# Kernel optimization log

Hardware: AMD Instinct MI355X
Metric: run time of the kernel (lower is better)

The kernel has to match this reference:

```python
import jax, jax.numpy as jnp
import numpy as np

N_TOKENS = 16384
MODEL_DIM = 2048
NUM_EXPERTS = 16
TOP_K = 2
CAPACITY_FACTOR = 1.0
NUM_SPLIT = 2  # os.environ 'num_split' default in source


def setup_inputs() -> dict:
    key = jax.random.key(0)
    kx, kw = jax.random.split(key)
    x = jax.random.normal(kx, (N_TOKENS, MODEL_DIM), dtype=jnp.float32)
    # kaiming_normal_ on Linear weight: std = sqrt(2 / fan_in)
    wg = jax.random.normal(kw, (NUM_EXPERTS, MODEL_DIM), dtype=jnp.float32) * np.float32(np.sqrt(2.0 / MODEL_DIM))
    return {"x": x, "wg": wg}


def _loss_compute(logits):
    gates = jax.nn.softmax(logits, axis=1)              # [N, E]
    num_experts = logits.shape[1]
    indices1_s = jnp.argmax(gates, axis=1)              # [N]
    mask1 = jax.nn.one_hot(indices1_s, num_experts, dtype=gates.dtype)
    me = jnp.mean(gates, axis=0)
    ce = jnp.mean(mask1, axis=0)
    l_aux = jnp.sum(me * ce) * num_experts
    return l_aux, indices1_s, gates


def _dispatch_fix_capacity(gates, k, capacity_factor, num_split):
    # gates is detached in the original (torch .detach())
    gates = jax.lax.stop_gradient(gates)
    n, e = gates.shape
    capacity = int(k * n // e * capacity_factor) // num_split * num_split
    values, topk_idx = jax.lax.top_k(gates, k)          # [N, k]
    weights = values
    flat_experts = topk_idx.reshape(-1)                 # [N*k]
    order = jnp.argsort(flat_experts)                   # stable sort by expert id
    experts_sorted = flat_experts[order]
    token_ids = jnp.repeat(jnp.arange(n, dtype=jnp.int32), k)[order]
    # position of each routed token within its expert's run
    counts = jax.ops.segment_sum(jnp.ones_like(flat_experts, dtype=jnp.int32), flat_experts, num_segments=e)
    starts = jnp.cumsum(counts) - counts                # exclusive prefix sum
    pos = jnp.arange(n * k, dtype=jnp.int32) - starts[experts_sorted]
    # fixed-capacity index table, -1 = empty slot; overflow tokens dropped
    ind = jnp.full((e, capacity), -1, dtype=jnp.int32)
    ind = ind.at[experts_sorted, pos].set(token_ids, mode="drop")  # pos>=capacity dropped
    indices = ind.reshape(-1)                           # [E*capacity], expert-major
    mask = indices >= 0
    expert_ids = jnp.repeat(jnp.arange(e, dtype=gates.dtype), capacity)
    return weights, indices, expert_ids, mask


def reference(x, wg):
    logits = jnp.einsum("nd,ed->ne", x, wg)             # Linear, no bias
    l_aux, _indices1, gates = _loss_compute(logits)
    weights, indices, expert_ids, mask = _dispatch_fix_capacity(
        gates, TOP_K, CAPACITY_FACTOR, NUM_SPLIT)
    return l_aux, weights, indices, expert_ids
```

## Files before the change

### kernel.cpp

```cpp
#include <hip/hip_runtime.h>
#include <hip/hip_bf16.h>
#include <stdint.h>

#define N_TOKENS    16384
#define MODEL_DIM   2048
#define NUM_EXPERTS 16
#define CAPACITY    2048
#define NBLK2       512
#define NBLK        256
#define GBLK        512
#define W_OFF       1
#define IDX_OFF     (1 + 2 * N_TOKENS)
#define EID_OFF     (IDX_OFF + NUM_EXPERTS * CAPACITY)

#define SC_E01    0
#define SC_CNTH   16384
#define SC_CEH    32768
#define SC_START  49152
#define SC_TOT    57344
#define SC_ME     57408

#define DPPX(v, ctrl) __int_as_float(__builtin_amdgcn_update_dpp(             \
    0, __float_as_int(v), (ctrl), 0xF, 0xF, true))
#define SWZ(v, off) __int_as_float(__builtin_amdgcn_ds_swizzle(               \
    __float_as_int(v), (off)))

__global__ __launch_bounds__(512) void k_logits(
    const float* __restrict__ x, const float* __restrict__ wg,
    float* __restrict__ out, uint8_t* __restrict__ ws)
{
  __shared__ float part[8][32][17];
  const int tid = threadIdx.x;
  const int b = blockIdx.x;
  const int l = tid & 63;
  const int kr = tid >> 6;
  const int kb = kr * 256 + l * 4;

  float4 w[16];
#pragma unroll
  for (int e = 0; e < NUM_EXPERTS; ++e)
    w[e] = *reinterpret_cast<const float4*>(wg + e * MODEL_DIM + kb);

  const float* xp = x + (size_t)(b * 32) * MODEL_DIM + kb;
  float4 xva = *reinterpret_cast<const float4*>(xp);

  const bool h0 = l & 1, h1 = l & 2, h2 = l & 4, h3 = l & 8;

  for (int t = 0; t < 32; ++t) {
    float4 xvb;
    if (t < 31)
      xvb = *reinterpret_cast<const float4*>(xp + (size_t)(t + 1) * MODEL_DIM);

    float cur[16];
#pragma unroll
    for (int e = 0; e < NUM_EXPERTS; ++e)
      cur[e] = xva.x * w[e].x + xva.y * w[e].y + xva.z * w[e].z + xva.w * w[e].w;

#pragma unroll
    for (int r = 0; r < 8; ++r) {
      float k = h0 ? cur[2 * r + 1] : cur[2 * r];
      float o = h0 ? cur[2 * r]     : cur[2 * r + 1];
      cur[r] = k + DPPX(o, 0xB1);
    }
#pragma unroll
    for (int r = 0; r < 4; ++r) {
      float k = h1 ? cur[2 * r + 1] : cur[2 * r];
      float o = h1 ? cur[2 * r]     : cur[2 * r + 1];
      cur[r] = k + DPPX(o, 0x4E);
    }
#pragma unroll
    for (int r = 0; r < 2; ++r) {
      float k = h2 ? cur[2 * r + 1] : cur[2 * r];
      float o = h2 ? cur[2 * r]     : cur[2 * r + 1];
      cur[r] = k + SWZ(o, 0x101F);
    }
    float v;
    {
      float k = h3 ? cur[1] : cur[0];
      float o = h3 ? cur[0] : cur[1];
      v = k + SWZ(o, 0x201F);
    }
    v += SWZ(v, 0x401F);
    v += __shfl_xor(v, 32, 64);
    if (l < NUM_EXPERTS) part[kr][t][l] = v;
    xva = xvb;
  }
  __syncthreads();

  if (tid < 32) {
    const int tg = b * 32 + tid;
    float logit[NUM_EXPERTS];
#pragma unroll
    for (int e = 0; e < NUM_EXPERTS; ++e) {
      float s = part[0][tid][e];
#pragma unroll
      for (int k2 = 1; k2 < 8; ++k2) s += part[k2][tid][e];
      logit[e] = s;
    }

    float m = logit[0];
#pragma unroll
    for (int e = 1; e < NUM_EXPERTS; e++) m = fmaxf(m, logit[e]);
    float gg[NUM_EXPERTS]; float z = 0.f;
#pragma unroll
    for (int e = 0; e < NUM_EXPERTS; e++) { gg[e] = expf(logit[e] - m); z += gg[e]; }
    float inv = 1.f / z;
#pragma unroll
    for (int e = 0; e < NUM_EXPERTS; e++) gg[e] *= inv;

    float v1 = gg[0], v2 = -1.f; int e1 = 0, e2 = 0;
#pragma unroll
    for (int e = 1; e < NUM_EXPERTS; e++) {
      if (gg[e] > v1) { v2 = v1; e2 = e1; v1 = gg[e]; e1 = e; }
      else if (gg[e] > v2) { v2 = gg[e]; e2 = e; }
    }
    out[W_OFF + 2 * tg]     = v1;
    out[W_OFF + 2 * tg + 1] = v2;
    ws[SC_E01 + tg] = (uint8_t)(e1 | (e2 << 4));

    int mycount = 0, myce = 0;
    for (int e = 0; e < NUM_EXPERTS; e++) {
      unsigned long long m1 = __ballot(e1 == e);
      unsigned long long m2 = __ballot(e2 == e);
      if (tid == e) { mycount = __popcll(m1 | m2); myce = __popcll(m1); }
    }
    if (tid < NUM_EXPERTS) {
      reinterpret_cast<uint16_t*>(ws + SC_CNTH)[tid * NBLK2 + b] = (uint16_t)mycount;
      reinterpret_cast<uint16_t*>(ws + SC_CEH)[tid * NBLK2 + b] = (uint16_t)myce;
    }

#pragma unroll
    for (int e = 0; e < NUM_EXPERTS; e++) {
      gg[e] += __shfl_xor(gg[e], 1, 64);
      gg[e] += __shfl_xor(gg[e], 2, 64);
      gg[e] += __shfl_xor(gg[e], 4, 64);
      gg[e] += __shfl_xor(gg[e], 8, 64);
      gg[e] += __shfl_xor(gg[e], 16, 64);
    }
    if (tid == 0) {
      float* mp = reinterpret_cast<float*>(ws + SC_ME);
#pragma unroll
      for (int e = 0; e < NUM_EXPERTS; e++) mp[b * NUM_EXPERTS + e] = gg[e];
    }
  }
}

__global__ __launch_bounds__(256) void k_finish(
    uint8_t* __restrict__ ws, float* __restrict__ out) {
  const uint16_t* cnth = reinterpret_cast<const uint16_t*>(ws + SC_CNTH);
  uint16_t* starts = reinterpret_cast<uint16_t*>(ws + SC_START);
  uint16_t* totw = reinterpret_cast<uint16_t*>(ws + SC_TOT);
  __shared__ int gs[NUM_EXPERTS][16];
  __shared__ int gstart[NUM_EXPERTS][17];
  __shared__ float sme[NUM_EXPERTS][17];
  __shared__ int sce[NUM_EXPERTS][17];
  const int tid = threadIdx.x;
  const int e = tid >> 4, grp = tid & 15;
  int s = 0;
  for (int hc = grp * 32; hc < grp * 32 + 32; hc++) s += cnth[e * NBLK2 + hc];
  gs[e][grp] = s;
  {
    const float* mepart = reinterpret_cast<const float*>(ws + SC_ME);
    const uint16_t* ceh = reinterpret_cast<const uint16_t*>(ws + SC_CEH);
    float ms = 0.f; int cs = 0;
    for (int k = grp; k < NBLK2; k += 16) {
      ms += mepart[k * NUM_EXPERTS + e];
      cs += ceh[e * NBLK2 + k];
    }
    sme[e][grp] = ms; sce[e][grp] = cs;
  }
  __syncthreads();
  if (tid < NUM_EXPERTS) {
    int run = 0;
    for (int g2 = 0; g2 < 16; g2++) { gstart[tid][g2] = run; run += gs[tid][g2]; }
  }
  __syncthreads();
  int run = gstart[e][grp];
  for (int c = grp * 16; c < grp * 16 + 16; c++) {
    starts[e * NBLK + c] = (uint16_t)run;
    run += cnth[e * NBLK2 + 2 * c] + cnth[e * NBLK2 + 2 * c + 1];
  }
  if (grp == 15) totw[e] = (uint16_t)run;
  if (tid < NUM_EXPERTS) {
    float ssum = 0.f; int ce = 0;
    for (int g2 = 0; g2 < 16; g2++) { ssum += sme[tid][g2]; ce += sce[tid][g2]; }
    float prod = (ssum * (1.0f / N_TOKENS)) * ((float)ce * (1.0f / N_TOKENS));
    prod += __shfl_xor(prod, 1, 64);
    prod += __shfl_xor(prod, 2, 64);
    prod += __shfl_xor(prod, 4, 64);
    prod += __shfl_xor(prod, 8, 64);
    if (tid == 0) out[0] = prod * (float)NUM_EXPERTS;
  }
}

__global__ __launch_bounds__(192) void k_scatter_fill(
    const uint8_t* __restrict__ ws, float* __restrict__ out) {
  const uint16_t* starts = reinterpret_cast<const uint16_t*>(ws + SC_START);
  const uint16_t* totw = reinterpret_cast<const uint16_t*>(ws + SC_TOT);
  const int tid = threadIdx.x;
  const int b = blockIdx.x;
  if (tid < 64) {
    const int t = b * 64 + tid;
    const int v = ws[SC_E01 + t];
    const int e1 = v & 15, e2 = v >> 4;
    const unsigned long long below = (1ull << tid) - 1ull;
    int p1 = CAPACITY, p2 = CAPACITY;
    for (int e = 0; e < NUM_EXPERTS; e++) {
      unsigned long long m = __ballot(e1 == e) | __ballot(e2 == e);
      int r = __popcll(m & below);
      int sbase = (int)starts[e * NBLK + b];
      if (e1 == e) p1 = sbase + r;
      if (e2 == e) p2 = sbase + r;
    }
    float tf = (float)t;
    if ((unsigned)p1 < (unsigned)CAPACITY) out[IDX_OFF + e1 * CAPACITY + p1] = tf;
    if ((unsigned)p2 < (unsigned)CAPACITY) out[IDX_OFF + e2 * CAPACITY + p2] = tf;
  } else {
    const int slot = b * 128 + (tid - 64);
    const int e = slot >> 11;
    const int p = slot & (CAPACITY - 1);
    if (p >= (int)totw[e]) out[IDX_OFF + slot] = -1.0f;
    out[EID_OFF + slot] = (float)e;
  }
}

extern "C" void kernel_launch(void* const* d_in, const int* in_sizes, int n_in,
                              void* d_out, int out_size, void* d_ws, size_t ws_size,
                              hipStream_t stream) {
  const float* x  = (const float*)d_in[0];
  const float* wg = (const float*)d_in[1];
  float* out = (float*)d_out;
  uint8_t* ws = (uint8_t*)d_ws;

  k_logits<<<GBLK, 512, 0, stream>>>(x, wg, out, ws);
  k_finish<<<1, 256, 0, stream>>>(ws, out);
  k_scatter_fill<<<NBLK, 192, 0, stream>>>(ws, out);
}
```

Before: 52.11 us.

## Fuse finish into scatter kernel with per-block prefix recompute, deepen x prefetch

Removes the single-block k_finish launch. Each scatter block now recomputes its own per-expert exclusive prefix and totals from the histogram counts, and an extra block 256 computes the aux loss. This cuts a kernel launch and a serial dependency stage, at the cost of redundant histogram reads in every block. The logits kernel also prefetches x two rows ahead instead of one, and replaces one ds_swizzle with a DPP row-shift for the cross-8-lane reduction step.

```diff
diff --git a/kernel.cpp b/kernel.cpp
--- a/kernel.cpp
+++ b/kernel.cpp
@@ -16,9 +16,7 @@
 #define SC_E01    0
 #define SC_CNTH   16384
 #define SC_CEH    32768
-#define SC_START  49152
-#define SC_TOT    57344
-#define SC_ME     57408
+#define SC_ME     49152
 
 #define DPPX(v, ctrl) __int_as_float(__builtin_amdgcn_update_dpp(             \
     0, __float_as_int(v), (ctrl), 0xF, 0xF, true))
@@ -43,13 +41,14 @@
 
   const float* xp = x + (size_t)(b * 32) * MODEL_DIM + kb;
   float4 xva = *reinterpret_cast<const float4*>(xp);
+  float4 xvb = *reinterpret_cast<const float4*>(xp + MODEL_DIM);
 
   const bool h0 = l & 1, h1 = l & 2, h2 = l & 4, h3 = l & 8;
 
   for (int t = 0; t < 32; ++t) {
-    float4 xvb;
-    if (t < 31)
-      xvb = *reinterpret_cast<const float4*>(xp + (size_t)(t + 1) * MODEL_DIM);
+    float4 xvc;
+    if (t < 30)
+      xvc = *reinterpret_cast<const float4*>(xp + (size_t)(t + 2) * MODEL_DIM);
 
     float cur[16];
 #pragma unroll
@@ -78,12 +77,12 @@
     {
       float k = h3 ? cur[1] : cur[0];
       float o = h3 ? cur[0] : cur[1];
-      v = k + SWZ(o, 0x201F);
+      v = k + DPPX(o, 0x128);
     }
     v += SWZ(v, 0x401F);
     v += __shfl_xor(v, 32, 64);
     if (l < NUM_EXPERTS) part[kr][t][l] = v;
-    xva = xvb;
+    xva = xvb; xvb = xvc;
   }
   __syncthreads();
 
@@ -145,60 +144,58 @@
   }
 }
 
-__global__ __launch_bounds__(256) void k_finish(
-    uint8_t* __restrict__ ws, float* __restrict__ out) {
-  const uint16_t* cnth = reinterpret_cast<const uint16_t*>(ws + SC_CNTH);
-  uint16_t* starts = reinterpret_cast<uint16_t*>(ws + SC_START);
-  uint16_t* totw = reinterpret_cast<uint16_t*>(ws + SC_TOT);
-  __shared__ int gs[NUM_EXPERTS][16];
-  __shared__ int gstart[NUM_EXPERTS][17];
-  __shared__ float sme[NUM_EXPERTS][17];
-  __shared__ int sce[NUM_EXPERTS][17];
-  const int tid = threadIdx.x;
-  const int e = tid >> 4, grp = tid & 15;
-  int s = 0;
-  for (int hc = grp * 32; hc < grp * 32 + 32; hc++) s += cnth[e * NBLK2 + hc];
-  gs[e][grp] = s;
-  {
-    const float* mepart = reinterpret_cast<const float*>(ws + SC_ME);
-    const uint16_t* ceh = reinterpret_cast<const uint16_t*>(ws + SC_CEH);
-    float ms = 0.f; int cs = 0;
-    for (int k = grp; k < NBLK2; k += 16) {
-      ms += mepart[k * NUM_EXPERTS + e];
-      cs += ceh[e * NBLK2 + k];
-    }
-    sme[e][grp] = ms; sce[e][grp] = cs;
-  }
-  __syncthreads();
-  if (tid < NUM_EXPERTS) {
-    int run = 0;
-    for (int g2 = 0; g2 < 16; g2++) { gstart[tid][g2] = run; run += gs[tid][g2]; }
-  }
-  __syncthreads();
-  int run = gstart[e][grp];
-  for (int c = grp * 16; c < grp * 16 + 16; c++) {
-    starts[e * NBLK + c] = (uint16_t)run;
-    run += cnth[e * NBLK2 + 2 * c] + cnth[e * NBLK2 + 2 * c + 1];
-  }
-  if (grp == 15) totw[e] = (uint16_t)run;
-  if (tid < NUM_EXPERTS) {
-    float ssum = 0.f; int ce = 0;
-    for (int g2 = 0; g2 < 16; g2++) { ssum += sme[tid][g2]; ce += sce[tid][g2]; }
-    float prod = (ssum * (1.0f / N_TOKENS)) * ((float)ce * (1.0f / N_TOKENS));
-    prod += __shfl_xor(prod, 1, 64);
-    prod += __shfl_xor(prod, 2, 64);
-    prod += __shfl_xor(prod, 4, 64);
-    prod += __shfl_xor(prod, 8, 64);
-    if (tid == 0) out[0] = prod * (float)NUM_EXPERTS;
-  }
-}
-
-__global__ __launch_bounds__(192) void k_scatter_fill(
+__global__ __launch_bounds__(192) void k_tail(
     const uint8_t* __restrict__ ws, float* __restrict__ out) {
-  const uint16_t* starts = reinterpret_cast<const uint16_t*>(ws + SC_START);
-  const uint16_t* totw = reinterpret_cast<const uint16_t*>(ws + SC_TOT);
+  __shared__ int sstart[NUM_EXPERTS];
+  __shared__ int stot[NUM_EXPERTS];
   const int tid = threadIdx.x;
   const int b = blockIdx.x;
+
+  if (b == 256) {
+    __shared__ float sme2[12][NUM_EXPERTS];
+    __shared__ int sce2[12][NUM_EXPERTS];
+    const float* me = reinterpret_cast<const float*>(ws + SC_ME);
+    const uint16_t* ceh = reinterpret_cast<const uint16_t*>(ws + SC_CEH);
+    const int e = tid & 15, grp = tid >> 4;
+    float ms = 0.f; int cs = 0;
+    for (int k = grp; k < NBLK2; k += 12) {
+      ms += me[k * NUM_EXPERTS + e];
+      cs += ceh[e * NBLK2 + k];
+    }
+    sme2[grp][e] = ms; sce2[grp][e] = cs;
+    __syncthreads();
+    if (tid < NUM_EXPERTS) {
+      float ssum = 0.f; int ce = 0;
+#pragma unroll
+      for (int g2 = 0; g2 < 12; g2++) { ssum += sme2[g2][tid]; ce += sce2[g2][tid]; }
+      float prod = (ssum * (1.0f / N_TOKENS)) * ((float)ce * (1.0f / N_TOKENS));
+      prod += __shfl_xor(prod, 1, 64);
+      prod += __shfl_xor(prod, 2, 64);
+      prod += __shfl_xor(prod, 4, 64);
+      prod += __shfl_xor(prod, 8, 64);
+      if (tid == 0) out[0] = prod * (float)NUM_EXPERTS;
+    }
+    return;
+  }
+
+  if (tid < 64) {
+    const int e = tid >> 2, q = tid & 3;
+    const uint32_t* row =
+        reinterpret_cast<const uint32_t*>(ws + SC_CNTH) + e * (NBLK2 / 2) + q * 64;
+    const int limit = 2 * b;
+    int s_lt = 0, s_all = 0;
+    for (int wd = 0; wd < 64; ++wd) {
+      uint32_t v = row[wd];
+      int pair = (int)(v & 0xFFFF) + (int)(v >> 16);
+      s_all += pair;
+      if (q * 128 + 2 * wd < limit) s_lt += pair;
+    }
+    s_lt += __shfl_xor(s_lt, 1, 64);  s_lt += __shfl_xor(s_lt, 2, 64);
+    s_all += __shfl_xor(s_all, 1, 64); s_all += __shfl_xor(s_all, 2, 64);
+    if (q == 0) { sstart[e] = s_lt; stot[e] = s_all; }
+  }
+  __syncthreads();
+
   if (tid < 64) {
     const int t = b * 64 + tid;
     const int v = ws[SC_E01 + t];
@@ -208,7 +205,7 @@
     for (int e = 0; e < NUM_EXPERTS; e++) {
       unsigned long long m = __ballot(e1 == e) | __ballot(e2 == e);
       int r = __popcll(m & below);
-      int sbase = (int)starts[e * NBLK + b];
+      int sbase = sstart[e];
       if (e1 == e) p1 = sbase + r;
       if (e2 == e) p2 = sbase + r;
     }
@@ -219,7 +216,7 @@
     const int slot = b * 128 + (tid - 64);
     const int e = slot >> 11;
     const int p = slot & (CAPACITY - 1);
-    if (p >= (int)totw[e]) out[IDX_OFF + slot] = -1.0f;
+    if (p >= stot[e]) out[IDX_OFF + slot] = -1.0f;
     out[EID_OFF + slot] = (float)e;
   }
 }
@@ -233,6 +230,5 @@
   uint8_t* ws = (uint8_t*)d_ws;
 
   k_logits<<<GBLK, 512, 0, stream>>>(x, wg, out, ws);
-  k_finish<<<1, 256, 0, stream>>>(ws, out);
-  k_scatter_fill<<<NBLK, 192, 0, stream>>>(ws, out);
+  k_tail<<<257, 192, 0, stream>>>(ws, out);
 }
```

Result: faster. 49.79 us (-4.4%).
